# Optimization experiments

Hardware: AMD Instinct MI355X
Metric: run time of the kernel (lower is better)

Reference implementation:

```python
import jax, jax.numpy as jnp
import numpy as np

D_MODEL, D_STATE, EXPAND, D_CONV = 96, 16, 2, 3
D_INNER = EXPAND * D_MODEL  # 192
DT_RANK = -(-D_MODEL // 16)  # 6
K = 4
B, H, W = 4, 64, 64


def setup_inputs() -> dict:
    key = jax.random.key(0)
    ks = jax.random.split(key, 12)
    x = jax.random.normal(ks[0], (B, H, W, D_MODEL), jnp.float32)
    in_proj_w = jax.random.normal(ks[1], (2 * D_INNER, D_MODEL), jnp.float32) * 0.02
    conv_w = jax.random.normal(ks[2], (D_INNER, 1, D_CONV, D_CONV), jnp.float32) * 0.1
    conv_b = jnp.zeros((D_INNER,), jnp.float32)
    x_proj_w = jax.random.normal(ks[3], (K, DT_RANK + 2 * D_STATE, D_INNER), jnp.float32) * 0.02
    dt_proj_w = jax.random.uniform(ks[4], (K, D_INNER, DT_RANK), jnp.float32,
                                   -DT_RANK ** -0.5, DT_RANK ** -0.5)
    dt = jnp.exp(jax.random.uniform(ks[5], (K, D_INNER)) *
                 (np.log(0.1) - np.log(0.001)) + np.log(0.001))
    dt = jnp.clip(dt, 1e-4, None)
    dt_proj_b = dt + jnp.log(-jnp.expm1(-dt))  # inverse-softplus init
    A_logs = jnp.tile(jnp.log(jnp.arange(1, D_STATE + 1, dtype=jnp.float32))[None, :],
                      (K * D_INNER, 1))
    Ds = jnp.ones((K * D_INNER,), jnp.float32)
    norm_g = jnp.ones((D_INNER,), jnp.float32)
    norm_b = jnp.zeros((D_INNER,), jnp.float32)
    out_proj_w = jax.random.normal(ks[6], (D_MODEL, D_INNER), jnp.float32) * 0.02
    return dict(x=x, in_proj_w=in_proj_w, conv_w=conv_w, conv_b=conv_b,
                x_proj_w=x_proj_w, dt_proj_w=dt_proj_w, dt_proj_b=dt_proj_b,
                A_logs=A_logs, Ds=Ds, norm_g=norm_g, norm_b=norm_b,
                out_proj_w=out_proj_w)


def _selective_scan(u, delta, A, Bmat, Cmat, Dvec):
    # u,delta: (B,K,D,L)  A: (K,D,N)  Bmat,Cmat: (B,K,N,L)  Dvec: (K,D)
    uT = jnp.moveaxis(u, -1, 0)      # (L,B,K,D)
    dT = jnp.moveaxis(delta, -1, 0)  # (L,B,K,D)
    BT = jnp.moveaxis(Bmat, -1, 0)   # (L,B,K,N)
    CT = jnp.moveaxis(Cmat, -1, 0)   # (L,B,K,N)
    h0 = jnp.zeros(u.shape[:3] + (A.shape[-1],), u.dtype)  # (B,K,D,N)

    def step(h, inp):
        u_t, d_t, B_t, C_t = inp
        dA = jnp.exp(d_t[..., None] * A)                       # (B,K,D,N)
        dBu = (d_t * u_t)[..., None] * B_t[..., None, :]       # (B,K,D,N)
        h = dA * h + dBu
        y = jnp.sum(h * C_t[..., None, :], axis=-1)            # (B,K,D)
        return h, y

    _, ys = jax.lax.scan(step, h0, (uT, dT, BT, CT))
    y = jnp.moveaxis(ys, 0, -1)  # (B,K,D,L)
    return y + Dvec[None, :, :, None] * u


def reference(x, in_proj_w, conv_w, conv_b, x_proj_w, dt_proj_w, dt_proj_b,
              A_logs, Ds, norm_g, norm_b, out_proj_w):
    Bn, Hn, Wn, _ = x.shape
    L = Hn * Wn
    xz = x @ in_proj_w.T                       # (B,H,W,2*Dinner)
    xi, z = jnp.split(xz, 2, axis=-1)
    xi = jnp.transpose(xi, (0, 3, 1, 2))       # (B,Dinner,H,W)
    xi = jax.lax.conv_general_dilated(xi, conv_w, (1, 1), 'SAME',
                                      feature_group_count=D_INNER,
                                      dimension_numbers=('NCHW', 'OIHW', 'NCHW'))
    xi = xi + conv_b[None, :, None, None]
    xi = jax.nn.silu(xi)

    # 4 scan directions
    x_hw = xi.reshape(Bn, D_INNER, L)
    x_wh = jnp.transpose(xi, (0, 1, 3, 2)).reshape(Bn, D_INNER, L)
    x_hwwh = jnp.stack([x_hw, x_wh], axis=1)               # (B,2,D,L)
    xs = jnp.concatenate([x_hwwh, jnp.flip(x_hwwh, axis=-1)], axis=1)  # (B,4,D,L)

    x_dbl = jnp.einsum('bkdl,kcd->bkcl', xs, x_proj_w)
    dts, Bs, Cs = jnp.split(x_dbl, [DT_RANK, DT_RANK + D_STATE], axis=2)
    dts = jnp.einsum('bkrl,kdr->bkdl', dts, dt_proj_w)
    delta = jax.nn.softplus(dts + dt_proj_b[None, :, :, None])

    A = -jnp.exp(A_logs).reshape(K, D_INNER, D_STATE)
    Dv = Ds.reshape(K, D_INNER)
    out_y = _selective_scan(xs, delta, A, Bs, Cs, Dv)       # (B,4,D,L)

    inv_y = jnp.flip(out_y[:, 2:4], axis=-1)                # (B,2,D,L)
    wh_y = jnp.transpose(out_y[:, 1].reshape(Bn, D_INNER, Wn, Hn),
                         (0, 1, 3, 2)).reshape(Bn, D_INNER, L)
    invwh_y = jnp.transpose(inv_y[:, 1].reshape(Bn, D_INNER, Wn, Hn),
                            (0, 1, 3, 2)).reshape(Bn, D_INNER, L)
    y = out_y[:, 0] + inv_y[:, 0] + wh_y + invwh_y          # (B,D,L)

    y = jnp.transpose(y, (0, 2, 1)).reshape(Bn, Hn, Wn, D_INNER)
    mu = jnp.mean(y, axis=-1, keepdims=True)
    var = jnp.var(y, axis=-1, keepdims=True)
    y = (y - mu) * jax.lax.rsqrt(var + 1e-5) * norm_g + norm_b
    y = y * jax.nn.silu(z)
    return y @ out_proj_w.T
```

## Files before the change

### kernel.cpp

```cpp
#include <hip/hip_runtime.h>
#include <math.h>

#define BN 4
#define LL 4096
#define DM 96
#define DI 192
#define NS 16
#define KK 4
#define RR 6
#define NCH 64
#define LC (LL/NCH)

__device__ __forceinline__ float silu_f(float x){ return x / (1.f + __expf(-x)); }
__device__ __forceinline__ float softplus_f(float x){
  return (x > 20.f) ? x : log1pf(__expf(x));
}
__device__ __forceinline__ void fma4(float4& a, const float4 w, const float4 v){
  a.x = fmaf(w.x, v.x, a.x); a.y = fmaf(w.y, v.y, a.y);
  a.z = fmaf(w.z, v.z, a.z); a.w = fmaf(w.w, v.w, a.w);
}

__global__ __launch_bounds__(256) void k1_inproj(const float* __restrict__ x,
    const float* __restrict__ w, float* __restrict__ xi, float* __restrict__ zs)
{
  __shared__ float xt[16][DM];
  __shared__ float wt[64][DM+4];
  int blk = blockIdx.x;
  int b = blk >> 8;
  int l0 = (blk & 255) << 4;
  int tid = threadIdx.x;
  for (int idx = tid; idx < 16*24; idx += 256) {
    int t = idx / 24, jj = idx % 24;
    ((float4*)xt[t])[jj] = *(const float4*)(x + ((size_t)(b*LL + l0 + t))*DM + 4*jj);
  }
  int cl = tid & 63;
  int tb = (tid >> 6) * 4;
  for (int ct = 0; ct < 6; ++ct) {
    int c0 = ct*64;
    __syncthreads();
    for (int idx = tid; idx < 64*24; idx += 256) {
      int r = idx / 24, jj = idx % 24;
      ((float4*)wt[r])[jj] = *(const float4*)(w + (size_t)(c0 + r)*DM + 4*jj);
    }
    __syncthreads();
    float4 a0={0,0,0,0}, a1={0,0,0,0}, a2={0,0,0,0}, a3={0,0,0,0};
    const float4* wr = (const float4*)wt[cl];
    const float4* x0 = (const float4*)xt[tb+0];
    const float4* x1 = (const float4*)xt[tb+1];
    const float4* x2 = (const float4*)xt[tb+2];
    const float4* x3 = (const float4*)xt[tb+3];
    #pragma unroll
    for (int jj = 0; jj < 24; ++jj) {
      float4 w4 = wr[jj];
      fma4(a0, w4, x0[jj]); fma4(a1, w4, x1[jj]);
      fma4(a2, w4, x2[jj]); fma4(a3, w4, x3[jj]);
    }
    float accs[4] = { (a0.x+a0.y)+(a0.z+a0.w), (a1.x+a1.y)+(a1.z+a1.w),
                      (a2.x+a2.y)+(a2.z+a2.w), (a3.x+a3.y)+(a3.z+a3.w) };
    int c = c0 + cl;
    #pragma unroll
    for (int tt = 0; tt < 4; ++tt) {
      int l = l0 + tb + tt;
      float v = accs[tt];
      if (c < DI) xi[((size_t)(b*LL + l))*DI + c] = v;
      else        zs[((size_t)(b*LL + l))*DI + (c - DI)] = silu_f(v);
    }
  }
}

__global__ __launch_bounds__(256) void k2_conv(const float* __restrict__ xi,
    const float* __restrict__ cw, const float* __restrict__ cb,
    float* __restrict__ U0, float* __restrict__ U1)
{
  int n = blockIdx.x*256 + threadIdx.x;
  if (n >= BN*LL*48) return;
  int c4 = n % 48;
  int w_ = (n / 48) & 63;
  int h_ = (n / (48*64)) & 63;
  int b  = n / (48*LL);
  int c  = c4 * 4;
  float4 acc = { cb[c], cb[c+1], cb[c+2], cb[c+3] };
  #pragma unroll
  for (int kh = 0; kh < 3; ++kh) {
    int hh = h_ + kh - 1;
    if (hh < 0 || hh >= 64) continue;
    #pragma unroll
    for (int kw = 0; kw < 3; ++kw) {
      int ww2 = w_ + kw - 1;
      if (ww2 < 0 || ww2 >= 64) continue;
      float4 v = *(const float4*)(xi + ((size_t)(b*LL) + hh*64 + ww2)*DI + c);
      int tap = kh*3 + kw;
      acc.x = fmaf(v.x, cw[(c+0)*9 + tap], acc.x);
      acc.y = fmaf(v.y, cw[(c+1)*9 + tap], acc.y);
      acc.z = fmaf(v.z, cw[(c+2)*9 + tap], acc.z);
      acc.w = fmaf(v.w, cw[(c+3)*9 + tap], acc.w);
    }
  }
  float4 o = { silu_f(acc.x), silu_f(acc.y), silu_f(acc.z), silu_f(acc.w) };
  *(float4*)(U0 + ((size_t)(b*LL) + h_*64 + w_)*DI + c) = o;
  *(float4*)(U1 + ((size_t)(b*LL) + w_*64 + h_)*DI + c) = o;
}

__global__ __launch_bounds__(256) void k3_xproj(const float* __restrict__ U0,
    const float* __restrict__ U1, const float* __restrict__ xw,
    const float* __restrict__ dtw, const float* __restrict__ dtb,
    float* __restrict__ dlt, float* __restrict__ BCs)
{
  __shared__ float ut[16][DI];
  __shared__ float xwS[38][DI+4];
  __shared__ float c38S[16][38];
  __shared__ float dtwS[DI*RR];
  int blk = blockIdx.x;
  int tile = blk & 255; int k = (blk >> 8) & 3; int b = blk >> 10;
  int l0 = tile << 4;
  int tid = threadIdx.x;
  const float* U = (k & 1) ? U1 : U0;
  for (int idx = tid; idx < 16*48; idx += 256) {
    int t = idx / 48, jj = idx % 48;
    ((float4*)ut[t])[jj] = *(const float4*)(U + ((size_t)(b*LL + l0 + t))*DI + 4*jj);
  }
  for (int idx = tid; idx < 38*48; idx += 256) {
    int r = idx / 48, jj = idx % 48;
    ((float4*)xwS[r])[jj] = *(const float4*)(xw + (size_t)(k*38 + r)*DI + 4*jj);
  }
  for (int idx = tid; idx < DI*RR; idx += 256)
    dtwS[idx] = dtw[k*DI*RR + idx];
  __syncthreads();
  for (int idx = tid; idx < 16*38; idx += 256) {
    int t = idx / 38, cc = idx % 38;
    const float4* u4 = (const float4*)ut[t];
    const float4* w4 = (const float4*)xwS[cc];
    float4 a4 = {0,0,0,0};
    #pragma unroll
    for (int jj = 0; jj < 48; ++jj) fma4(a4, u4[jj], w4[jj]);
    float acc = (a4.x+a4.y)+(a4.z+a4.w);
    c38S[t][cc] = acc;
    if (cc >= RR) BCs[(((size_t)(b*KK + k)*LL) + l0 + t)*32 + (cc - RR)] = acc;
  }
  __syncthreads();
  for (int idx = tid; idx < 16*DI; idx += 256) {
    int t = idx / DI, d = idx % DI;
    float acc = dtb[k*DI + d];
    #pragma unroll
    for (int r = 0; r < RR; ++r) acc += c38S[t][r] * dtwS[d*RR + r];
    dlt[(((size_t)(b*KK + k)*LL) + l0 + t)*DI + d] = softplus_f(acc);
  }
}

__device__ __forceinline__ void pow_tree(float e1, float* ep){
  ep[0]=e1;
  ep[1]=e1*e1;
  ep[2]=ep[1]*e1;  ep[3]=ep[1]*ep[1];
  ep[4]=ep[3]*e1;  ep[5]=ep[3]*ep[1]; ep[6]=ep[3]*ep[2]; ep[7]=ep[3]*ep[3];
  #pragma unroll
  for (int i=0;i<8;++i) ep[8+i]=ep[7]*ep[i];
}

__global__ __launch_bounds__(192) void k4a_pass1(const float* __restrict__ dlt,
    const float* __restrict__ U0, const float* __restrict__ U1,
    const float* __restrict__ BCs, const float* __restrict__ A_logs,
    float* __restrict__ hst, float* __restrict__ Ssum)
{
  int blk = blockIdx.x;
  int c = blk % NCH; int k = (blk / NCH) & 3; int b = blk / (NCH*4);
  int d = threadIdx.x;
  const float* U = (k & 1) ? U1 : U0;
  int b4k = b*KK + k;
  float an[NS];
  #pragma unroll
  for (int n = 0; n < NS; ++n) an[n] = -__expf(A_logs[(k*DI + d)*NS + n]);
  float a0 = an[0];
  bool chain = true;
  #pragma unroll
  for (int n = 1; n < NS; ++n)
    chain = chain && (fabsf(an[n] - a0*(float)(n+1)) <= 1e-3f*(float)(n+1));
  float h[NS];
  #pragma unroll
  for (int n = 0; n < NS; ++n) h[n] = 0.f;
  float sd = 0.f;
  bool fwd = (k < 2);
  int lo = c * LC;
  int dir = fwd ? 1 : -1;
  int l = fwd ? lo : (lo + LC - 1);
  const float* pd = dlt + ((size_t)b4k*LL + l)*DI + d;
  const float* pu = U + ((size_t)(b*LL) + l)*DI + d;
  const float4* pbc = (const float4*)(BCs + ((size_t)b4k*LL + l)*32);
  intptr_t pinc = (intptr_t)dir * DI;
  intptr_t bcinc = (intptr_t)dir * 8;
  #pragma unroll 2
  for (int s = 0; s < LC; ++s) {
    float dv = *pd;
    float u  = *pu;
    float du = dv * u;
    sd += dv;
    float4 B0 = pbc[0], B1 = pbc[1], B2 = pbc[2], B3 = pbc[3];
    float Bv[NS] = {B0.x,B0.y,B0.z,B0.w, B1.x,B1.y,B1.z,B1.w,
                    B2.x,B2.y,B2.z,B2.w, B3.x,B3.y,B3.z,B3.w};
    if (chain) {
      float ep[NS];
      pow_tree(__expf(a0 * dv), ep);
      #pragma unroll
      for (int n = 0; n < NS; ++n) h[n] = fmaf(ep[n], h[n], du*Bv[n]);
    } else {
      #pragma unroll
      for (int n = 0; n < NS; ++n) h[n] = fmaf(__expf(an[n]*dv), h[n], du*Bv[n]);
    }
    pd += pinc; pu += pinc; pbc += bcinc;
  }
  size_t base = ((size_t)b4k*NCH + c)*DI + d;
  float4* he = (float4*)(hst + base*NS);
  he[0] = make_float4(h[0], h[1], h[2], h[3]);
  he[1] = make_float4(h[4], h[5], h[6], h[7]);
  he[2] = make_float4(h[8], h[9], h[10],h[11]);
  he[3] = make_float4(h[12],h[13],h[14],h[15]);
  Ssum[base] = sd;
}

__global__ __launch_bounds__(256) void k4b_combine(float* __restrict__ hst,
    const float* __restrict__ Ssum, const float* __restrict__ A_logs)
{
  int blk = blockIdx.x;
  int dgrp = blk % 12; int k = (blk/12) & 3; int b = blk/48;
  int tid = threadIdx.x;
  int d = dgrp*16 + (tid >> 4);
  int n = tid & 15;
  int b4k = b*KK + k;
  float an = -__expf(A_logs[(k*DI + d)*NS + n]);
  bool fwd = (k < 2);
  float h = 0.f;
  for (int s = 0; s < NCH; ++s) {
    int c = fwd ? s : (NCH - 1 - s);
    size_t base = ((size_t)b4k*NCH + c)*DI + d;
    float he = hst[base*NS + n];
    hst[base*NS + n] = h;
    h = __expf(an * Ssum[base]) * h + he;
  }
}

__global__ __launch_bounds__(192) void k4c_pass2(const float* __restrict__ dlt,
    const float* __restrict__ U0, const float* __restrict__ U1,
    const float* __restrict__ BCs, const float* __restrict__ A_logs,
    const float* __restrict__ Dsv, const float* __restrict__ hst,
    float* __restrict__ ytot)
{
  int blk = blockIdx.x;
  int c = blk % NCH; int k = (blk / NCH) & 3; int b = blk / (NCH*4);
  int d = threadIdx.x;
  const float* U = (k & 1) ? U1 : U0;
  int b4k = b*KK + k;
  float an[NS];
  #pragma unroll
  for (int n = 0; n < NS; ++n) an[n] = -__expf(A_logs[(k*DI + d)*NS + n]);
  float a0 = an[0];
  bool chain = true;
  #pragma unroll
  for (int n = 1; n < NS; ++n)
    chain = chain && (fabsf(an[n] - a0*(float)(n+1)) <= 1e-3f*(float)(n+1));
  float Dd = Dsv[k*DI + d];
  size_t base = ((size_t)b4k*NCH + c)*DI + d;
  float h[NS];
  {
    const float4* hi = (const float4*)(hst + base*NS);
    float4 h0 = hi[0], h1 = hi[1], h2 = hi[2], h3 = hi[3];
    h[0]=h0.x; h[1]=h0.y; h[2]=h0.z; h[3]=h0.w;
    h[4]=h1.x; h[5]=h1.y; h[6]=h1.z; h[7]=h1.w;
    h[8]=h2.x; h[9]=h2.y; h[10]=h2.z; h[11]=h2.w;
    h[12]=h3.x; h[13]=h3.y; h[14]=h3.z; h[15]=h3.w;
  }
  bool fwd = (k < 2);
  int lo = c * LC;
  int dir = fwd ? 1 : -1;
  int l = fwd ? lo : (lo + LC - 1);
  const float* pd = dlt + ((size_t)b4k*LL + l)*DI + d;
  const float* pu = U + ((size_t)(b*LL) + l)*DI + d;
  const float4* pbc = (const float4*)(BCs + ((size_t)b4k*LL + l)*32);
  intptr_t pinc = (intptr_t)dir * DI;
  intptr_t bcinc = (intptr_t)dir * 8;
  bool odd = (k & 1);
  #pragma unroll 2
  for (int s = 0; s < LC; ++s) {
    float dv = *pd;
    float u  = *pu;
    float du = dv * u;
    float4 B0 = pbc[0], B1 = pbc[1], B2 = pbc[2], B3 = pbc[3];
    float4 C0 = pbc[4], C1 = pbc[5], C2 = pbc[6], C3 = pbc[7];
    float Bv[NS] = {B0.x,B0.y,B0.z,B0.w, B1.x,B1.y,B1.z,B1.w,
                    B2.x,B2.y,B2.z,B2.w, B3.x,B3.y,B3.z,B3.w};
    float Cv[NS] = {C0.x,C0.y,C0.z,C0.w, C1.x,C1.y,C1.z,C1.w,
                    C2.x,C2.y,C2.z,C2.w, C3.x,C3.y,C3.z,C3.w};
    if (chain) {
      float ep[NS];
      pow_tree(__expf(a0 * dv), ep);
      #pragma unroll
      for (int n = 0; n < NS; ++n) h[n] = fmaf(ep[n], h[n], du*Bv[n]);
    } else {
      #pragma unroll
      for (int n = 0; n < NS; ++n) h[n] = fmaf(__expf(an[n]*dv), h[n], du*Bv[n]);
    }
    float p0 = Dd*u, p1 = 0.f, p2 = 0.f, p3 = 0.f;
    #pragma unroll
    for (int n = 0; n < NS; n += 4) {
      p0 = fmaf(h[n+0], Cv[n+0], p0);
      p1 = fmaf(h[n+1], Cv[n+1], p1);
      p2 = fmaf(h[n+2], Cv[n+2], p2);
      p3 = fmaf(h[n+3], Cv[n+3], p3);
    }
    int pos = odd ? (((l & 63) << 6) | (l >> 6)) : l;
    unsafeAtomicAdd(&ytot[((size_t)(b*LL) + pos)*DI + d], (p0+p1)+(p2+p3));
    l += dir; pd += pinc; pu += pinc; pbc += bcinc;
  }
}

__global__ __launch_bounds__(384) void k5_final(const float* __restrict__ ytot,
    const float* __restrict__ zs, const float* __restrict__ g,
    const float* __restrict__ bb, const float* __restrict__ ow,
    float* __restrict__ out)
{
  __shared__ float yt[32][DI+4];
  __shared__ float muS[32], rsS[32];
  int blk = blockIdx.x;
  int b = blk >> 7; int l0 = (blk & 127) << 5;
  int tid = threadIdx.x;
  for (int idx = tid; idx < 32*48; idx += 384) {
    int r = idx / 48, jj = idx % 48;
    ((float4*)yt[r])[jj] = *(const float4*)(ytot + ((size_t)(b*LL) + l0 + r)*DI + 4*jj);
  }
  __syncthreads();
  if (tid < 256) {
    int r = tid >> 3, q = tid & 7;
    const float* row = yt[r];
    float s1 = 0.f, s2 = 0.f;
    #pragma unroll
    for (int i = 0; i < 24; ++i) {
      float v = row[q*24 + i];
      s1 += v; s2 += v*v;
    }
    s1 += __shfl_xor(s1, 1); s2 += __shfl_xor(s2, 1);
    s1 += __shfl_xor(s1, 2); s2 += __shfl_xor(s2, 2);
    s1 += __shfl_xor(s1, 4); s2 += __shfl_xor(s2, 4);
    if (q == 0) {
      float mu = s1 / (float)DI;
      float var = s2 / (float)DI - mu*mu;
      muS[r] = mu;
      rsS[r] = rsqrtf(var + 1e-5f);
    }
  }
  __syncthreads();
  for (int idx = tid; idx < 32*48; idx += 384) {
    int r = idx / 48, jj = idx % 48;
    float4 y = ((float4*)yt[r])[jj];
    float mu = muS[r], rs = rsS[r];
    float4 g4 = *(const float4*)(g + 4*jj);
    float4 b4 = *(const float4*)(bb + 4*jj);
    float4 z4 = *(const float4*)(zs + ((size_t)(b*LL) + l0 + r)*DI + 4*jj);
    float4 v;
    v.x = fmaf((y.x-mu)*rs, g4.x, b4.x) * z4.x;
    v.y = fmaf((y.y-mu)*rs, g4.y, b4.y) * z4.y;
    v.z = fmaf((y.z-mu)*rs, g4.z, b4.z) * z4.z;
    v.w = fmaf((y.w-mu)*rs, g4.w, b4.w) * z4.w;
    ((float4*)yt[r])[jj] = v;
  }
  __syncthreads();
  {
    int c = tid % 96;
    int rg = tid / 96;
    const float4* wrow = (const float4*)(ow + (size_t)c*DI);
    float4 acc[8];
    #pragma unroll
    for (int rr = 0; rr < 8; ++rr) acc[rr] = make_float4(0.f,0.f,0.f,0.f);
    #pragma unroll
    for (int ch = 0; ch < 6; ++ch) {
      float4 wreg[8];
      #pragma unroll
      for (int jj = 0; jj < 8; ++jj) wreg[jj] = wrow[ch*8 + jj];
      #pragma unroll
      for (int rr = 0; rr < 8; ++rr) {
        const float4* yr = (const float4*)yt[rg*8 + rr];
        #pragma unroll
        for (int jj = 0; jj < 8; ++jj) fma4(acc[rr], wreg[jj], yr[ch*8 + jj]);
      }
    }
    #pragma unroll
    for (int rr = 0; rr < 8; ++rr) {
      float v = (acc[rr].x+acc[rr].y)+(acc[rr].z+acc[rr].w);
      out[((size_t)(b*LL) + l0 + rg*8 + rr)*DM + c] = v;
    }
  }
}

extern "C" void kernel_launch(void* const* d_in, const int* in_sizes, int n_in,
                              void* d_out, int out_size, void* d_ws, size_t ws_size,
                              hipStream_t stream)
{
  const float* x    = (const float*)d_in[0];
  const float* ipw  = (const float*)d_in[1];
  const float* cw   = (const float*)d_in[2];
  const float* cb   = (const float*)d_in[3];
  const float* xpw  = (const float*)d_in[4];
  const float* dtwp = (const float*)d_in[5];
  const float* dtbp = (const float*)d_in[6];
  const float* alog = (const float*)d_in[7];
  const float* dsp  = (const float*)d_in[8];
  const float* ng   = (const float*)d_in[9];
  const float* nbp  = (const float*)d_in[10];
  const float* owp  = (const float*)d_in[11];
  float* out = (float*)d_out;

  float* ws = (float*)d_ws;
  size_t off = 0;
  float* ytot = ws + off; off += (size_t)BN*LL*DI;
  float* zs   = ws + off; off += (size_t)BN*LL*DI;
  float* xi   = ws + off; off += (size_t)BN*LL*DI;
  float* U0   = ws + off; off += (size_t)BN*LL*DI;
  float* U1   = ws + off; off += (size_t)BN*LL*DI;
  float* dlt  = ws + off; off += (size_t)BN*KK*LL*DI;
  float* BCs  = ws + off; off += (size_t)BN*KK*LL*32;
  float* hst  = ws + off; off += (size_t)BN*KK*NCH*DI*NS;
  float* Ssum = ws + off; off += (size_t)BN*KK*NCH*DI;
  (void)ws_size; (void)in_sizes; (void)n_in; (void)out_size;

  hipMemsetAsync(ytot, 0, (size_t)BN*LL*DI*sizeof(float), stream);
  k1_inproj<<<dim3(BN*256), dim3(256), 0, stream>>>(x, ipw, xi, zs);
  k2_conv<<<dim3((BN*LL*48 + 255)/256), dim3(256), 0, stream>>>(xi, cw, cb, U0, U1);
  k3_xproj<<<dim3(BN*KK*256), dim3(256), 0, stream>>>(U0, U1, xpw, dtwp, dtbp, dlt, BCs);
  k4a_pass1<<<dim3(BN*KK*NCH), dim3(192), 0, stream>>>(dlt, U0, U1, BCs, alog, hst, Ssum);
  k4b_combine<<<dim3(BN*KK*12), dim3(256), 0, stream>>>(hst, Ssum, alog);
  k4c_pass2<<<dim3(BN*KK*NCH), dim3(192), 0, stream>>>(dlt, U0, U1, BCs, alog, dsp, hst, ytot);
  k5_final<<<dim3(BN*128), dim3(384), 0, stream>>>(ytot, zs, ng, nbp, owp, out);
}
```

Before: 405.5 us.

## Fuse delta projection and softplus into scan passes, drop delta buffer

The x-projection kernel no longer computes and stores the full per-channel delta tensor (B*K*L*192 floats). It writes only the six dt-rank values next to B and C in a 40-wide row. Both scan passes then recompute delta per step from those values with a per-thread dt_proj weight row and a numerically stable softplus. This removes a large global write and two large reads in exchange for extra ALU work (a 6-term dot product plus exp and log, done twice). The x-projection kernel is also retiled to 32 rows with a transposed weight layout in shared memory, so each thread computes 4 rows.

```diff
diff --git a/kernel.cpp b/kernel.cpp
--- a/kernel.cpp
+++ b/kernel.cpp
@@ -10,10 +10,11 @@
 #define RR 6
 #define NCH 64
 #define LC (LL/NCH)
+#define BCW 40
 
 __device__ __forceinline__ float silu_f(float x){ return x / (1.f + __expf(-x)); }
 __device__ __forceinline__ float softplus_f(float x){
-  return (x > 20.f) ? x : log1pf(__expf(x));
+  return fmaxf(x, 0.f) + __logf(1.f + __expf(-fabsf(x)));
 }
 __device__ __forceinline__ void fma4(float4& a, const float4 w, const float4 v){
   a.x = fmaf(w.x, v.x, a.x); a.y = fmaf(w.y, v.y, a.y);
@@ -101,49 +102,55 @@
   *(float4*)(U1 + ((size_t)(b*LL) + w_*64 + h_)*DI + c) = o;
 }
 
-__global__ __launch_bounds__(256) void k3_xproj(const float* __restrict__ U0,
+__global__ __launch_bounds__(320) void k3_xproj(const float* __restrict__ U0,
     const float* __restrict__ U1, const float* __restrict__ xw,
-    const float* __restrict__ dtw, const float* __restrict__ dtb,
-    float* __restrict__ dlt, float* __restrict__ BCs)
-{
-  __shared__ float ut[16][DI];
-  __shared__ float xwS[38][DI+4];
-  __shared__ float c38S[16][38];
-  __shared__ float dtwS[DI*RR];
-  int blk = blockIdx.x;
-  int tile = blk & 255; int k = (blk >> 8) & 3; int b = blk >> 10;
-  int l0 = tile << 4;
+    float* __restrict__ BC)
+{
+  __shared__ float  ut[32][DI];
+  __shared__ float4 wT[48][41];
+  __shared__ float  cS[32][BCW];
+  int blk = blockIdx.x;
+  int tile = blk & 127; int k = (blk >> 7) & 3; int b = blk >> 9;
+  int l0 = tile << 5;
   int tid = threadIdx.x;
   const float* U = (k & 1) ? U1 : U0;
-  for (int idx = tid; idx < 16*48; idx += 256) {
-    int t = idx / 48, jj = idx % 48;
-    ((float4*)ut[t])[jj] = *(const float4*)(U + ((size_t)(b*LL + l0 + t))*DI + 4*jj);
-  }
-  for (int idx = tid; idx < 38*48; idx += 256) {
+  int b4k = b*KK + k;
+  for (int idx = tid; idx < 32*48; idx += 320) {
     int r = idx / 48, jj = idx % 48;
-    ((float4*)xwS[r])[jj] = *(const float4*)(xw + (size_t)(k*38 + r)*DI + 4*jj);
-  }
-  for (int idx = tid; idx < DI*RR; idx += 256)
-    dtwS[idx] = dtw[k*DI*RR + idx];
+    ((float4*)ut[r])[jj] = *(const float4*)(U + ((size_t)(b*LL + l0 + r))*DI + 4*jj);
+  }
+  for (int idx = tid; idx < 38*48; idx += 320) {
+    int cc = idx / 48, jj = idx % 48;
+    wT[jj][cc] = *(const float4*)(xw + (size_t)(k*38 + cc)*DI + 4*jj);
+  }
   __syncthreads();
-  for (int idx = tid; idx < 16*38; idx += 256) {
-    int t = idx / 38, cc = idx % 38;
-    const float4* u4 = (const float4*)ut[t];
-    const float4* w4 = (const float4*)xwS[cc];
-    float4 a4 = {0,0,0,0};
-    #pragma unroll
-    for (int jj = 0; jj < 48; ++jj) fma4(a4, u4[jj], w4[jj]);
-    float acc = (a4.x+a4.y)+(a4.z+a4.w);
-    c38S[t][cc] = acc;
-    if (cc >= RR) BCs[(((size_t)(b*KK + k)*LL) + l0 + t)*32 + (cc - RR)] = acc;
+  int cc = tid % 40;
+  int rg = tid / 40;
+  if (cc < 38) {
+    float4 a0={0,0,0,0}, a1={0,0,0,0}, a2={0,0,0,0}, a3={0,0,0,0};
+    const float4* u0 = (const float4*)ut[rg*4+0];
+    const float4* u1 = (const float4*)ut[rg*4+1];
+    const float4* u2 = (const float4*)ut[rg*4+2];
+    const float4* u3 = (const float4*)ut[rg*4+3];
+    #pragma unroll
+    for (int jj = 0; jj < 48; ++jj) {
+      float4 w4 = wT[jj][cc];
+      fma4(a0, w4, u0[jj]); fma4(a1, w4, u1[jj]);
+      fma4(a2, w4, u2[jj]); fma4(a3, w4, u3[jj]);
+    }
+    int cp = (cc < RR) ? (32 + cc) : (cc - RR);
+    cS[rg*4+0][cp] = (a0.x+a0.y)+(a0.z+a0.w);
+    cS[rg*4+1][cp] = (a1.x+a1.y)+(a1.z+a1.w);
+    cS[rg*4+2][cp] = (a2.x+a2.y)+(a2.z+a2.w);
+    cS[rg*4+3][cp] = (a3.x+a3.y)+(a3.z+a3.w);
+  } else {
+    cS[rg*4+0][cc] = 0.f; cS[rg*4+1][cc] = 0.f;
+    cS[rg*4+2][cc] = 0.f; cS[rg*4+3][cc] = 0.f;
   }
   __syncthreads();
-  for (int idx = tid; idx < 16*DI; idx += 256) {
-    int t = idx / DI, d = idx % DI;
-    float acc = dtb[k*DI + d];
-    #pragma unroll
-    for (int r = 0; r < RR; ++r) acc += c38S[t][r] * dtwS[d*RR + r];
-    dlt[(((size_t)(b*KK + k)*LL) + l0 + t)*DI + d] = softplus_f(acc);
+  {
+    int r = tid / 10, q = tid % 10;
+    *(float4*)(BC + ((size_t)b4k*LL + l0 + r)*BCW + 4*q) = ((float4*)cS[r])[q];
   }
 }
 
@@ -156,9 +163,21 @@
   for (int i=0;i<8;++i) ep[8+i]=ep[7]*ep[i];
 }
 
-__global__ __launch_bounds__(192) void k4a_pass1(const float* __restrict__ dlt,
-    const float* __restrict__ U0, const float* __restrict__ U1,
-    const float* __restrict__ BCs, const float* __restrict__ A_logs,
+__device__ __forceinline__ float delta_of(const float* __restrict__ row,
+    const float* __restrict__ dw, float dtb1){
+  float4 t4 = *(const float4*)(row + 32);
+  float2 t2 = *(const float2*)(row + 36);
+  float a = dtb1;
+  a = fmaf(t4.x, dw[0], a); a = fmaf(t4.y, dw[1], a);
+  a = fmaf(t4.z, dw[2], a); a = fmaf(t4.w, dw[3], a);
+  a = fmaf(t2.x, dw[4], a); a = fmaf(t2.y, dw[5], a);
+  return softplus_f(a);
+}
+
+__global__ __launch_bounds__(192) void k4a_pass1(const float* __restrict__ U0,
+    const float* __restrict__ U1, const float* __restrict__ BC,
+    const float* __restrict__ A_logs, const float* __restrict__ dtw,
+    const float* __restrict__ dtb,
     float* __restrict__ hst, float* __restrict__ Ssum)
 {
   int blk = blockIdx.x;
@@ -174,6 +193,10 @@
   #pragma unroll
   for (int n = 1; n < NS; ++n)
     chain = chain && (fabsf(an[n] - a0*(float)(n+1)) <= 1e-3f*(float)(n+1));
+  float dw[RR];
+  #pragma unroll
+  for (int r = 0; r < RR; ++r) dw[r] = dtw[(k*DI + d)*RR + r];
+  float dtb1 = dtb[k*DI + d];
   float h[NS];
   #pragma unroll
   for (int n = 0; n < NS; ++n) h[n] = 0.f;
@@ -182,18 +205,18 @@
   int lo = c * LC;
   int dir = fwd ? 1 : -1;
   int l = fwd ? lo : (lo + LC - 1);
-  const float* pd = dlt + ((size_t)b4k*LL + l)*DI + d;
   const float* pu = U + ((size_t)(b*LL) + l)*DI + d;
-  const float4* pbc = (const float4*)(BCs + ((size_t)b4k*LL + l)*32);
+  const float* pbc = BC + ((size_t)b4k*LL + l)*BCW;
   intptr_t pinc = (intptr_t)dir * DI;
-  intptr_t bcinc = (intptr_t)dir * 8;
+  intptr_t bcinc = (intptr_t)dir * BCW;
   #pragma unroll 2
   for (int s = 0; s < LC; ++s) {
-    float dv = *pd;
+    float dv = delta_of(pbc, dw, dtb1);
     float u  = *pu;
     float du = dv * u;
     sd += dv;
-    float4 B0 = pbc[0], B1 = pbc[1], B2 = pbc[2], B3 = pbc[3];
+    const float4* b4p = (const float4*)pbc;
+    float4 B0 = b4p[0], B1 = b4p[1], B2 = b4p[2], B3 = b4p[3];
     float Bv[NS] = {B0.x,B0.y,B0.z,B0.w, B1.x,B1.y,B1.z,B1.w,
                     B2.x,B2.y,B2.z,B2.w, B3.x,B3.y,B3.z,B3.w};
     if (chain) {
@@ -205,7 +228,7 @@
       #pragma unroll
       for (int n = 0; n < NS; ++n) h[n] = fmaf(__expf(an[n]*dv), h[n], du*Bv[n]);
     }
-    pd += pinc; pu += pinc; pbc += bcinc;
+    pu += pinc; pbc += bcinc;
   }
   size_t base = ((size_t)b4k*NCH + c)*DI + d;
   float4* he = (float4*)(hst + base*NS);
@@ -237,11 +260,11 @@
   }
 }
 
-__global__ __launch_bounds__(192) void k4c_pass2(const float* __restrict__ dlt,
-    const float* __restrict__ U0, const float* __restrict__ U1,
-    const float* __restrict__ BCs, const float* __restrict__ A_logs,
-    const float* __restrict__ Dsv, const float* __restrict__ hst,
-    float* __restrict__ ytot)
+__global__ __launch_bounds__(192) void k4c_pass2(const float* __restrict__ U0,
+    const float* __restrict__ U1, const float* __restrict__ BC,
+    const float* __restrict__ A_logs, const float* __restrict__ dtw,
+    const float* __restrict__ dtb, const float* __restrict__ Dsv,
+    const float* __restrict__ hst, float* __restrict__ ytot)
 {
   int blk = blockIdx.x;
   int c = blk % NCH; int k = (blk / NCH) & 3; int b = blk / (NCH*4);
@@ -256,6 +279,10 @@
   #pragma unroll
   for (int n = 1; n < NS; ++n)
     chain = chain && (fabsf(an[n] - a0*(float)(n+1)) <= 1e-3f*(float)(n+1));
+  float dw[RR];
+  #pragma unroll
+  for (int r = 0; r < RR; ++r) dw[r] = dtw[(k*DI + d)*RR + r];
+  float dtb1 = dtb[k*DI + d];
   float Dd = Dsv[k*DI + d];
   size_t base = ((size_t)b4k*NCH + c)*DI + d;
   float h[NS];
@@ -271,19 +298,19 @@
   int lo = c * LC;
   int dir = fwd ? 1 : -1;
   int l = fwd ? lo : (lo + LC - 1);
-  const float* pd = dlt + ((size_t)b4k*LL + l)*DI + d;
   const float* pu = U + ((size_t)(b*LL) + l)*DI + d;
-  const float4* pbc = (const float4*)(BCs + ((size_t)b4k*LL + l)*32);
+  const float* pbc = BC + ((size_t)b4k*LL + l)*BCW;
   intptr_t pinc = (intptr_t)dir * DI;
-  intptr_t bcinc = (intptr_t)dir * 8;
+  intptr_t bcinc = (intptr_t)dir * BCW;
   bool odd = (k & 1);
   #pragma unroll 2
   for (int s = 0; s < LC; ++s) {
-    float dv = *pd;
+    float dv = delta_of(pbc, dw, dtb1);
     float u  = *pu;
     float du = dv * u;
-    float4 B0 = pbc[0], B1 = pbc[1], B2 = pbc[2], B3 = pbc[3];
-    float4 C0 = pbc[4], C1 = pbc[5], C2 = pbc[6], C3 = pbc[7];
+    const float4* b4p = (const float4*)pbc;
+    float4 B0 = b4p[0], B1 = b4p[1], B2 = b4p[2], B3 = b4p[3];
+    float4 C0 = b4p[4], C1 = b4p[5], C2 = b4p[6], C3 = b4p[7];
     float Bv[NS] = {B0.x,B0.y,B0.z,B0.w, B1.x,B1.y,B1.z,B1.w,
                     B2.x,B2.y,B2.z,B2.w, B3.x,B3.y,B3.z,B3.w};
     float Cv[NS] = {C0.x,C0.y,C0.z,C0.w, C1.x,C1.y,C1.z,C1.w,
@@ -307,7 +334,7 @@
     }
     int pos = odd ? (((l & 63) << 6) | (l >> 6)) : l;
     unsafeAtomicAdd(&ytot[((size_t)(b*LL) + pos)*DI + d], (p0+p1)+(p2+p3));
-    l += dir; pd += pinc; pu += pinc; pbc += bcinc;
+    l += dir; pu += pinc; pbc += bcinc;
   }
 }
 
@@ -413,8 +440,7 @@
   float* xi   = ws + off; off += (size_t)BN*LL*DI;
   float* U0   = ws + off; off += (size_t)BN*LL*DI;
   float* U1   = ws + off; off += (size_t)BN*LL*DI;
-  float* dlt  = ws + off; off += (size_t)BN*KK*LL*DI;
-  float* BCs  = ws + off; off += (size_t)BN*KK*LL*32;
+  float* BC   = ws + off; off += (size_t)BN*KK*LL*BCW;
   float* hst  = ws + off; off += (size_t)BN*KK*NCH*DI*NS;
   float* Ssum = ws + off; off += (size_t)BN*KK*NCH*DI;
   (void)ws_size; (void)in_sizes; (void)n_in; (void)out_size;
@@ -422,9 +448,9 @@
   hipMemsetAsync(ytot, 0, (size_t)BN*LL*DI*sizeof(float), stream);
   k1_inproj<<<dim3(BN*256), dim3(256), 0, stream>>>(x, ipw, xi, zs);
   k2_conv<<<dim3((BN*LL*48 + 255)/256), dim3(256), 0, stream>>>(xi, cw, cb, U0, U1);
-  k3_xproj<<<dim3(BN*KK*256), dim3(256), 0, stream>>>(U0, U1, xpw, dtwp, dtbp, dlt, BCs);
-  k4a_pass1<<<dim3(BN*KK*NCH), dim3(192), 0, stream>>>(dlt, U0, U1, BCs, alog, hst, Ssum);
+  k3_xproj<<<dim3(BN*KK*128), dim3(320), 0, stream>>>(U0, U1, xpw, BC);
+  k4a_pass1<<<dim3(BN*KK*NCH), dim3(192), 0, stream>>>(U0, U1, BC, alog, dtwp, dtbp, hst, Ssum);
   k4b_combine<<<dim3(BN*KK*12), dim3(256), 0, stream>>>(hst, Ssum, alog);
-  k4c_pass2<<<dim3(BN*KK*NCH), dim3(192), 0, stream>>>(dlt, U0, U1, BCs, alog, dsp, hst, ytot);
+  k4c_pass2<<<dim3(BN*KK*NCH), dim3(192), 0, stream>>>(U0, U1, BC, alog, dtwp, dtbp, dsp, hst, ytot);
   k5_final<<<dim3(BN*128), dim3(384), 0, stream>>>(ytot, zs, ng, nbp, owp, out);
 }
```

Result: faster. 388.6 us (-4.2%).
